# Performance work log

Hardware: AMD Instinct MI355X
Metric: run time of the kernel (lower is better)

## Reference

```python
import jax, jax.numpy as jnp
import numpy as np

N_U, N_I, D = 8192, 8192, 128


def setup_inputs() -> dict:
    key = jax.random.key(0)
    k1, k2, k3, k4, k5 = jax.random.split(key, 5)
    h_u = jax.random.normal(k1, (N_U, D), dtype=jnp.float32)
    h_i = jax.random.normal(k2, (N_I, D), dtype=jnp.float32)
    ui_adj = jax.random.randint(k3, (N_U, N_I), 0, 2).astype(jnp.int32)
    # learned params: W is nn.Linear(d, d, bias=False) -> weight [d, d]; a is [2d]
    W = jax.random.normal(k4, (D, D), dtype=jnp.float32) * (1.0 / np.sqrt(D))
    a = jax.random.normal(k5, (2 * D,), dtype=jnp.float32) * 0.1
    return {"h_u": h_u, "h_i": h_i, "ui_adj": ui_adj, "W": W, "a": a}


def reference(h_u, h_i, ui_adj, W, a):
    # torch nn.Linear: x @ W.T
    Wu = h_u @ W.T                      # [N_u, d]
    Wi = h_i @ W.T                      # [N_i, d]
    d = Wu.shape[1]
    a1 = Wu @ a[:d]                     # [N_u]
    a2 = Wi @ a[d:]                     # [N_i]
    e = jax.nn.leaky_relu(a1[:, None] + a2[None, :], negative_slope=0.2)  # [N_u, N_i]
    adj = ui_adj != 0
    no_item = ~adj.any(axis=-1)         # rows with zero neighbors
    e = jnp.where(adj, e, -jnp.inf)
    # avoid all -inf rows (torch softmax -> NaN -> nan_to_num -> 0); use 0 logits then zero alpha
    e = jnp.where(no_item[:, None], 0.0, e)
    alpha = jax.nn.softmax(e, axis=-1)  # [N_u, N_i]
    alpha = jnp.where(no_item[:, None], 0.0, alpha)
    out = alpha @ Wi                    # [N_u, d]
    out = jnp.where(no_item[:, None], 0.0, out)
    return (out, alpha)
```

## Files before the change

### kernel.cpp

```cpp
#include <hip/hip_runtime.h>

#define NU 8192
#define NI 8192
#define DD 128

typedef float fx4 __attribute__((ext_vector_type(4)));
typedef int   ix4 __attribute__((ext_vector_type(4)));
typedef short bx8 __attribute__((ext_vector_type(8)));
typedef short sx4 __attribute__((ext_vector_type(4)));

__device__ __forceinline__ short f2bf(float f) {
  unsigned u = __float_as_uint(f);
  u = (u + 0x7FFFu + ((u >> 16) & 1u)) >> 16;
  return (short)u;
}
__device__ __forceinline__ float lrelu(float x) { return fmaxf(x, 0.2f * x); }

__global__ __launch_bounds__(256) void k_prep(
    const float* __restrict__ hU, const float* __restrict__ hI,
    const float* __restrict__ W, const float* __restrict__ a,
    float* __restrict__ a1, float* __restrict__ e1, float* __restrict__ e2,
    short* __restrict__ WiT, float* __restrict__ blkmax)
{
  __shared__ float Wl[128 * 128];
  __shared__ float vv[2][128];
  __shared__ float red[64];
  const int tid = threadIdx.x;
#pragma unroll
  for (int it = 0; it < 16; ++it) {
    int idx = it * 1024 + tid * 4;
    *(fx4*)(Wl + idx) = *(const fx4*)(W + idx);
  }
  __syncthreads();
  if (tid < 128) {
    float s1 = 0.f, s2 = 0.f;
    for (int k = 0; k < DD; ++k) {
      float w = Wl[k * 128 + tid];
      s1 += a[k] * w;
      s2 += a[DD + k] * w;
    }
    vv[0][tid] = s1; vv[1][tid] = s2;
  }
  __syncthreads();

  const int i0 = blockIdx.x * 64;
  {
    const int rg = tid & 15;
    const int kg = tid >> 4;
    const int r0 = i0 + rg * 4;
    const int k0 = kg * 8;
    float acc[4][8];
#pragma unroll
    for (int r = 0; r < 4; ++r)
#pragma unroll
      for (int c = 0; c < 8; ++c) acc[r][c] = 0.f;
    for (int j = 0; j < 128; j += 4) {
      fx4 wv8[8], hv[4];
#pragma unroll
      for (int c = 0; c < 8; ++c) wv8[c] = *(const fx4*)(Wl + (k0 + c) * 128 + j);
#pragma unroll
      for (int r = 0; r < 4; ++r) hv[r] = *(const fx4*)(hI + (size_t)(r0 + r) * DD + j);
#pragma unroll
      for (int r = 0; r < 4; ++r)
#pragma unroll
        for (int c = 0; c < 8; ++c)
          acc[r][c] += hv[r][0]*wv8[c][0] + hv[r][1]*wv8[c][1] + hv[r][2]*wv8[c][2] + hv[r][3]*wv8[c][3];
    }
#pragma unroll
    for (int c = 0; c < 8; ++c) {
      sx4 pk;
#pragma unroll
      for (int r = 0; r < 4; ++r) pk[r] = f2bf(acc[r][c]);
      *(sx4*)(WiT + (size_t)(k0 + c) * NI + r0) = pk;
    }
  }

  if (tid < 64) {
    const int row = i0 + tid;
    const fx4* hv = (const fx4*)(hU + (size_t)row * DD);
    const fx4* vq = (const fx4*)&vv[0][0];
    float s = 0.f;
#pragma unroll
    for (int q = 0; q < DD / 4; ++q) {
      fx4 hq = hv[q], vqq = vq[q];
      s += hq[0]*vqq[0] + hq[1]*vqq[1] + hq[2]*vqq[2] + hq[3]*vqq[3];
    }
    a1[row] = s;
  } else if (tid < 128) {
    const int row = i0 + (tid - 64);
    const fx4* hv = (const fx4*)(hI + (size_t)row * DD);
    const fx4* vq = (const fx4*)&vv[1][0];
    float s = 0.f;
#pragma unroll
    for (int q = 0; q < DD / 4; ++q) {
      fx4 hq = hv[q], vqq = vq[q];
      s += hq[0]*vqq[0] + hq[1]*vqq[1] + hq[2]*vqq[2] + hq[3]*vqq[3];
    }
    e1[row] = __expf(s);
    e2[row] = __expf(0.2f * s);
    red[tid - 64] = s;
  }
  __syncthreads();
  if (tid < 32) red[tid] = fmaxf(red[tid], red[tid + 32]);
  __syncthreads();
  if (tid < 16) red[tid] = fmaxf(red[tid], red[tid + 16]);
  __syncthreads();
  if (tid < 8)  red[tid] = fmaxf(red[tid], red[tid + 8]);
  __syncthreads();
  if (tid < 4)  red[tid] = fmaxf(red[tid], red[tid + 4]);
  __syncthreads();
  if (tid == 0)
    blkmax[blockIdx.x] = fmaxf(fmaxf(red[0], red[1]), fmaxf(red[2], red[3]));
}

__global__ void k_mx(const float* __restrict__ blkmax, float* __restrict__ mx) {
  __shared__ float r[128];
  const int tid = threadIdx.x;
  r[tid] = blkmax[tid];
  __syncthreads();
  for (int s = 64; s > 0; s >>= 1) {
    if (tid < s) r[tid] = fmaxf(r[tid], r[tid + s]);
    __syncthreads();
  }
  if (tid == 0) mx[0] = r[0];
}

__global__ __launch_bounds__(256, 6) void k_phaseA(
    const int* __restrict__ adj, const float* __restrict__ a1g,
    const float* __restrict__ e1g, const float* __restrict__ e2g,
    const float* __restrict__ mxp,
    fx4* __restrict__ kcons, unsigned* __restrict__ mask)
{
  const int row  = blockIdx.x;
  const int tid  = threadIdx.x;
  const int lane = tid & 63;
  const int wv   = tid >> 6;
  const size_t base = (size_t)row * NI;
  ix4 m[8];
#pragma unroll
  for (int q = 0; q < 8; ++q)
    m[q] = __builtin_nontemporal_load((const ix4*)(adj + base + q * 1024 + tid * 4));
  const float A  = a1g[row];
  const float C  = lrelu(A + mxp[0]);
  const float K1 = __expf(A - C);
  const float K2 = __expf(0.2f * A - C);
  const float T1 = __expf(-A);
  float s1 = 0.f, s2 = 0.f;
#pragma unroll
  for (int q = 0; q < 8; ++q) {
    const int i0 = q * 1024 + tid * 4;
    const fx4 E1 = *(const fx4*)(e1g + i0);
    const fx4 E2 = *(const fx4*)(e2g + i0);
    unsigned long long b[4];
#pragma unroll
    for (int e = 0; e < 4; ++e) {
      const bool mm  = (m[q][e] != 0);
      const bool sel = (E1[e] > T1);
      s1 += (mm && sel)  ? E1[e] : 0.f;
      s2 += (mm && !sel) ? E2[e] : 0.f;
      b[e] = __ballot(mm);
    }
    if (lane < 8) {
      unsigned w = 0u;
#pragma unroll
      for (int e = 0; e < 4; ++e) {
        unsigned x = (unsigned)((b[e] >> (lane * 8)) & 0xFFull);
        x = (x | (x << 12)) & 0x000F000Fu;
        x = (x | (x << 6))  & 0x03030303u;
        x = (x | (x << 3))  & 0x11111111u;
        w |= x << e;
      }
      mask[(size_t)row * 256 + q * 32 + wv * 8 + lane] = w;
    }
  }
  float ps = K1 * s1 + K2 * s2;
#pragma unroll
  for (int st = 1; st < 64; st <<= 1) ps += __shfl_xor(ps, st, 64);
  __shared__ float lp[4];
  if (lane == 0) lp[wv] = ps;
  __syncthreads();
  if (tid == 0) {
    const float l = lp[0] + lp[1] + lp[2] + lp[3];
    const float ri = (l > 0.f) ? (1.f / l) : 0.f;
    kcons[row] = (fx4){K1 * ri, K2 * ri, T1, ri};
  }
}

__global__ __launch_bounds__(512, 4) void k_big(
    const unsigned* __restrict__ mask, const fx4* __restrict__ kcons,
    const float* __restrict__ e1g, const float* __restrict__ e2g,
    const short* __restrict__ WiT, float* __restrict__ partial,
    float* __restrict__ alphap)
{
  __shared__ __align__(16) char lds[32768];
  const int tid  = threadIdx.x;
  const int lane = tid & 63;
  const int wv   = tid >> 6;
  const int wm   = wv & 3;
  const int wn2  = wv >> 2;
  const int uTile = (int)blockIdx.x >> 2;
  const int quar  = (int)blockIdx.x & 3;
  const int u0 = uTile * 64;
  const int ib = quar * 2048;
  const int lr = lane & 15, lg = lane >> 4;

  const int rowm = u0 + wm * 16 + lr;
  const fx4 kcm = kcons[rowm];
  const float K1m = kcm[0], K2m = kcm[1], T1m = kcm[2];
  const unsigned* mrow = mask + (size_t)rowm * 256 + quar * 64;

  const int srow0 = u0 + wv * 8;

  const int sd = tid >> 3;
  const int si = tid & 7;
  const short* g0 = WiT + (size_t)sd * NI + ib + si * 8;
  const short* g1 = WiT + (size_t)(sd + 64) * NI + ib + si * 8;
  const int swz = (si * 16) ^ ((sd & 7) << 4);
  const int w0 = sd * 128 + swz;
  const int w1 = (sd + 64) * 128 + swz;

  fx4 acc[4];
#pragma unroll
  for (int n = 0; n < 4; ++n) acc[n] = (fx4){0.f, 0.f, 0.f, 0.f};

  bx8 sA = *(const bx8*)g0;
  bx8 sB = *(const bx8*)g1;
  *(bx8*)(lds + w0) = sA;
  *(bx8*)(lds + w1) = sB;

  for (int c = 0; c < 32; ++c) {
    char* buf = lds + (c & 1) * 16384;
    const int nxt = ((c + 1) & 1) * 16384;
    if (c < 31) {
      sA = *(const bx8*)(g0 + (c + 1) * 64);
      sB = *(const bx8*)(g1 + (c + 1) * 64);
    }
    __syncthreads();

#pragma unroll
    for (int ks = 0; ks < 2; ++ks) {
      const int ksg = c * 2 + ks;
      const unsigned by = (mrow[ksg] >> (lg * 8)) & 0xFFu;
      const int io = ksg * 32 + lg * 8;
      const fx4 e1a = *(const fx4*)(e1g + ib + io);
      const fx4 e1b = *(const fx4*)(e1g + ib + io + 4);
      const fx4 e2a = *(const fx4*)(e2g + ib + io);
      const fx4 e2b = *(const fx4*)(e2g + ib + io + 4);
      bx8 af;
#pragma unroll
      for (int j = 0; j < 8; ++j) {
        const float e1v = (j < 4) ? e1a[j] : e1b[j - 4];
        const float e2v = (j < 4) ? e2a[j] : e2b[j - 4];
        const float val = (e1v > T1m) ? e1v * K1m : e2v * K2m;
        af[j] = ((by >> j) & 1u) ? f2bf(val) : (short)0;
      }
#pragma unroll
      for (int nf = 0; nf < 4; ++nf) {
        const int d = wn2 * 64 + nf * 16 + lr;
        const bx8 bf = *(const bx8*)(buf + d * 128 +
                        ((ks * 64 + lg * 16) ^ ((lr & 7) << 4)));
        acc[nf] = __builtin_amdgcn_mfma_f32_16x16x32_bf16(af, bf, acc[nf], 0, 0, 0);
      }
    }

    if ((c & 3) == 3) {
      const int col = (c - 3) * 64 + lane * 4;
      const fx4 se1 = *(const fx4*)(e1g + ib + col);
      const fx4 se2 = *(const fx4*)(e2g + ib + col);
      const int wix = quar * 64 + (col >> 5);
      const int sh  = (lane & 7) * 4;
#pragma unroll
      for (int r = 0; r < 8; ++r) {
        const int row = srow0 + r;
        const fx4 kr = kcons[row];
        const unsigned nib = (mask[(size_t)row * 256 + wix] >> sh) & 0xFu;
        fx4 o;
#pragma unroll
        for (int j = 0; j < 4; ++j) {
          const float val = (se1[j] > kr[2]) ? se1[j] * kr[0] : se2[j] * kr[1];
          o[j] = ((nib >> j) & 1u) ? val : 0.f;
        }
        *(fx4*)(alphap + (size_t)row * NI + ib + col) = o;
      }
    }

    if (c < 31) {
      *(bx8*)(lds + nxt + w0) = sA;
      *(bx8*)(lds + nxt + w1) = sB;
    }
  }

  float* pb = partial + (size_t)blockIdx.x * (64 * 128);
#pragma unroll
  for (int nf = 0; nf < 4; ++nf)
#pragma unroll
    for (int v = 0; v < 4; ++v)
      pb[(wm * 16 + lg * 4 + v) * 128 + wn2 * 64 + nf * 16 + lr] = acc[nf][v];
}

__global__ __launch_bounds__(512) void k_comb(
    const float* __restrict__ partial, float* __restrict__ outp)
{
  const int g = blockIdx.x * 512 + threadIdx.x;
  const int u = g >> 5;
  const int c4 = (g & 31) * 4;
  const int uTile = u >> 6, r = u & 63;
  const float* p0 = partial + ((size_t)uTile * 4) * 8192 + r * 128 + c4;
  fx4 s = *(const fx4*)p0;
#pragma unroll
  for (int q = 1; q < 4; ++q) {
    fx4 t = *(const fx4*)(p0 + (size_t)q * 8192);
    s[0] += t[0]; s[1] += t[1]; s[2] += t[2]; s[3] += t[3];
  }
  *(fx4*)(outp + (size_t)u * DD + c4) = s;
}

extern "C" void kernel_launch(void* const* d_in, const int* in_sizes, int n_in,
                              void* d_out, int out_size, void* d_ws, size_t ws_size,
                              hipStream_t stream) {
  (void)in_sizes; (void)n_in; (void)out_size; (void)ws_size;
  const float* h_u = (const float*)d_in[0];
  const float* h_i = (const float*)d_in[1];
  const int*   adj = (const int*)d_in[2];
  const float* W   = (const float*)d_in[3];
  const float* a   = (const float*)d_in[4];

  float* outp   = (float*)d_out;
  float* alphap = (float*)d_out + (size_t)NU * DD;

  char* ws = (char*)d_ws;
  float*    mx     = (float*)(ws + 1024);
  float*    blkmax = (float*)(ws + 2048);
  float*    a1     = (float*)(ws + 4096);
  float*    e1t    = (float*)(ws + 102400);
  float*    e2t    = (float*)(ws + 135168);
  short*    WiT    = (short*)(ws + 262144);
  unsigned* mask   = (unsigned*)(ws + 2359296);
  float*    part   = (float*)(ws + 11534336);
  fx4*      kcons  = (fx4*)(ws + 29360128);

  k_prep   <<<128,  256, 0, stream>>>(h_u, h_i, W, a, a1, e1t, e2t, WiT, blkmax);
  k_mx     <<<1,    128, 0, stream>>>(blkmax, mx);
  k_phaseA <<<NU,   256, 0, stream>>>(adj, a1, e1t, e2t, mx, kcons, mask);
  k_big    <<<512,  512, 0, stream>>>(mask, kcons, e1t, e2t, WiT, part, alphap);
  k_comb   <<<512,  512, 0, stream>>>(part, outp);
}
```

Before: 203.2 us.

## Write alpha directly in the row-softmax kernel instead of the GEMM kernel

Moves the alpha output write from the MFMA GEMM kernel into the per-row softmax kernel. That kernel keeps the per-element unnormalised probabilities in registers, sums them directly, then scales by the reciprocal and stores alpha. This takes the strided alpha stores, plus their mask and kcons re-reads, out of the GEMM loop. The cost is more register pressure in the row kernel, whose occupancy hint drops from 6 to 4.

```diff
diff --git a/kernel.cpp b/kernel.cpp
--- a/kernel.cpp
+++ b/kernel.cpp
@@ -125,11 +125,12 @@
   if (tid == 0) mx[0] = r[0];
 }
 
-__global__ __launch_bounds__(256, 6) void k_phaseA(
+__global__ __launch_bounds__(256, 4) void k_fuseA(
     const int* __restrict__ adj, const float* __restrict__ a1g,
     const float* __restrict__ e1g, const float* __restrict__ e2g,
     const float* __restrict__ mxp,
-    fx4* __restrict__ kcons, unsigned* __restrict__ mask)
+    fx4* __restrict__ kcons, unsigned* __restrict__ mask,
+    float* __restrict__ alphap)
 {
   const int row  = blockIdx.x;
   const int tid  = threadIdx.x;
@@ -145,7 +146,8 @@
   const float K1 = __expf(A - C);
   const float K2 = __expf(0.2f * A - C);
   const float T1 = __expf(-A);
-  float s1 = 0.f, s2 = 0.f;
+  fx4 p[8];
+  float ps = 0.f;
 #pragma unroll
   for (int q = 0; q < 8; ++q) {
     const int i0 = q * 1024 + tid * 4;
@@ -156,8 +158,10 @@
     for (int e = 0; e < 4; ++e) {
       const bool mm  = (m[q][e] != 0);
       const bool sel = (E1[e] > T1);
-      s1 += (mm && sel)  ? E1[e] : 0.f;
-      s2 += (mm && !sel) ? E2[e] : 0.f;
+      const float val = sel ? E1[e] * K1 : E2[e] * K2;
+      const float pv  = mm ? val : 0.f;
+      p[q][e] = pv;
+      ps += pv;
       b[e] = __ballot(mm);
     }
     if (lane < 8) {
@@ -173,24 +177,27 @@
       mask[(size_t)row * 256 + q * 32 + wv * 8 + lane] = w;
     }
   }
-  float ps = K1 * s1 + K2 * s2;
 #pragma unroll
   for (int st = 1; st < 64; st <<= 1) ps += __shfl_xor(ps, st, 64);
   __shared__ float lp[4];
   if (lane == 0) lp[wv] = ps;
   __syncthreads();
-  if (tid == 0) {
-    const float l = lp[0] + lp[1] + lp[2] + lp[3];
-    const float ri = (l > 0.f) ? (1.f / l) : 0.f;
-    kcons[row] = (fx4){K1 * ri, K2 * ri, T1, ri};
-  }
-}
-
-__global__ __launch_bounds__(512, 4) void k_big(
+  const float l  = lp[0] + lp[1] + lp[2] + lp[3];
+  const float ri = (l > 0.f) ? (1.f / l) : 0.f;
+#pragma unroll
+  for (int q = 0; q < 8; ++q) {
+    fx4 o;
+#pragma unroll
+    for (int e = 0; e < 4; ++e) o[e] = p[q][e] * ri;
+    *(fx4*)(alphap + base + q * 1024 + tid * 4) = o;
+  }
+  if (tid == 0) kcons[row] = (fx4){K1 * ri, K2 * ri, T1, ri};
+}
+
+__global__ __launch_bounds__(512, 4) void k_gemm(
     const unsigned* __restrict__ mask, const fx4* __restrict__ kcons,
     const float* __restrict__ e1g, const float* __restrict__ e2g,
-    const short* __restrict__ WiT, float* __restrict__ partial,
-    float* __restrict__ alphap)
+    const short* __restrict__ WiT, float* __restrict__ partial)
 {
   __shared__ __align__(16) char lds[32768];
   const int tid  = threadIdx.x;
@@ -209,8 +216,6 @@
   const float K1m = kcm[0], K2m = kcm[1], T1m = kcm[2];
   const unsigned* mrow = mask + (size_t)rowm * 256 + quar * 64;
 
-  const int srow0 = u0 + wv * 8;
-
   const int sd = tid >> 3;
   const int si = tid & 7;
   const short* g0 = WiT + (size_t)sd * NI + ib + si * 8;
@@ -260,27 +265,6 @@
         const bx8 bf = *(const bx8*)(buf + d * 128 +
                         ((ks * 64 + lg * 16) ^ ((lr & 7) << 4)));
         acc[nf] = __builtin_amdgcn_mfma_f32_16x16x32_bf16(af, bf, acc[nf], 0, 0, 0);
-      }
-    }
-
-    if ((c & 3) == 3) {
-      const int col = (c - 3) * 64 + lane * 4;
-      const fx4 se1 = *(const fx4*)(e1g + ib + col);
-      const fx4 se2 = *(const fx4*)(e2g + ib + col);
-      const int wix = quar * 64 + (col >> 5);
-      const int sh  = (lane & 7) * 4;
-#pragma unroll
-      for (int r = 0; r < 8; ++r) {
-        const int row = srow0 + r;
-        const fx4 kr = kcons[row];
-        const unsigned nib = (mask[(size_t)row * 256 + wix] >> sh) & 0xFu;
-        fx4 o;
-#pragma unroll
-        for (int j = 0; j < 4; ++j) {
-          const float val = (se1[j] > kr[2]) ? se1[j] * kr[0] : se2[j] * kr[1];
-          o[j] = ((nib >> j) & 1u) ? val : 0.f;
-        }
-        *(fx4*)(alphap + (size_t)row * NI + ib + col) = o;
       }
     }
 
@@ -339,9 +323,9 @@
   float*    part   = (float*)(ws + 11534336);
   fx4*      kcons  = (fx4*)(ws + 29360128);
 
-  k_prep   <<<128,  256, 0, stream>>>(h_u, h_i, W, a, a1, e1t, e2t, WiT, blkmax);
-  k_mx     <<<1,    128, 0, stream>>>(blkmax, mx);
-  k_phaseA <<<NU,   256, 0, stream>>>(adj, a1, e1t, e2t, mx, kcons, mask);
-  k_big    <<<512,  512, 0, stream>>>(mask, kcons, e1t, e2t, WiT, part, alphap);
-  k_comb   <<<512,  512, 0, stream>>>(part, outp);
-}
+  k_prep  <<<128,  256, 0, stream>>>(h_u, h_i, W, a, a1, e1t, e2t, WiT, blkmax);
+  k_mx    <<<1,    128, 0, stream>>>(blkmax, mx);
+  k_fuseA <<<NU,   256, 0, stream>>>(adj, a1, e1t, e2t, mx, kcons, mask, alphap);
+  k_gemm  <<<512,  512, 0, stream>>>(mask, kcons, e1t, e2t, WiT, part);
+  k_comb  <<<512,  512, 0, stream>>>(part, outp);
+}
```

Result: no change. 203.4 us (+0.1%).
